# Kernel optimization log

Measured on AMD Instinct MI355X. Metric: run time of the kernel, lower is better.

Reference implementation:

```python
import jax, jax.numpy as jnp
import numpy as np

FP8_MAX = 448.0  # max representable magnitude of float8_e4m3fn
SCALE_EPS = 1e-7


def setup_inputs() -> dict:
    key = jax.random.key(0)
    k1, k2, k3 = jax.random.split(key, 3)
    in_f, out_f = 2048, 2048
    x = jax.random.normal(k1, (4, 4096, in_f), dtype=jnp.float32)
    # weight is stored in fp8 in the torch module; materialize fp8-representable fp32 values
    w_fp32 = jax.random.normal(k2, (out_f, in_f), dtype=jnp.float32) * (1.0 / np.sqrt(in_f))
    weight = w_fp32.astype(jnp.float8_e4m3fn).astype(jnp.float32)
    weight_scale = jnp.ones((), dtype=jnp.float32)
    bound = 1.0 / np.sqrt(in_f)
    bias = jax.random.uniform(k3, (out_f,), dtype=jnp.float32, minval=-bound, maxval=bound)
    return {"x": x, "weight": weight, "weight_scale": weight_scale, "bias": bias}


def reference(x, weight, weight_scale, bias):
    # per-tensor dynamic fp8 quantization of the input (scale = absmax / 448)
    scale = jnp.maximum(jnp.max(jnp.abs(x)) / FP8_MAX, SCALE_EPS)
    x_q = (x / scale).astype(jnp.float8_e4m3fn).astype(jnp.float32)
    # dequantize weight (fp8 values stored as fp32 here) with its per-tensor scale
    w = weight * weight_scale
    # NOTE: faithful to the source, the output is NOT rescaled by the input scale
    # (the original forward drops input_scale after quantization).
    out = jnp.einsum('bsi,oi->bso', x_q, w) + bias
    return out
```

## Files before the change

kernel.cpp:

```cpp
#include <hip/hip_runtime.h>
#include <hip/hip_bf16.h>

typedef __attribute__((ext_vector_type(4))) float floatx4;
typedef __attribute__((ext_vector_type(8))) int   intx8;

#define FP8_MAX_F 448.0f
#define SCALE_EPS 1e-7f

__global__ void k_absmax(const float* __restrict__ x, unsigned* __restrict__ amax, int n4) {
    __shared__ float wmax[4];
    int tid = blockIdx.x * blockDim.x + threadIdx.x;
    int stride = gridDim.x * blockDim.x;
    const float4* x4 = (const float4*)x;
    float m = 0.f;
    for (int i = tid; i < n4; i += stride) {
        float4 v = x4[i];
        m = fmaxf(fmaxf(fabsf(v.x), fabsf(v.y)),
                  fmaxf(m, fmaxf(fabsf(v.z), fabsf(v.w))));
    }
    #pragma unroll
    for (int off = 32; off > 0; off >>= 1) m = fmaxf(m, __shfl_xor(m, off, 64));
    if ((threadIdx.x & 63) == 0) wmax[threadIdx.x >> 6] = m;
    __syncthreads();
    if (threadIdx.x == 0) {
        float t = fmaxf(fmaxf(wmax[0], wmax[1]), fmaxf(wmax[2], wmax[3]));
        atomicMax(amax, __float_as_uint(t));
    }
}

__global__ void k_quant_w(const float* __restrict__ w, int* __restrict__ wq, int n16) {
    int tid = blockIdx.x * blockDim.x + threadIdx.x;
    int stride = gridDim.x * blockDim.x;
    const float4* x4 = (const float4*)w;
    int4* q4 = (int4*)wq;
    for (int i = tid; i < n16; i += stride) {
        float4 v0 = x4[4*i], v1 = x4[4*i+1], v2 = x4[4*i+2], v3 = x4[4*i+3];
        int4 o;
        o.x = __builtin_amdgcn_cvt_pk_fp8_f32(v0.x, v0.y, 0, false);
        o.x = __builtin_amdgcn_cvt_pk_fp8_f32(v0.z, v0.w, o.x, true);
        o.y = __builtin_amdgcn_cvt_pk_fp8_f32(v1.x, v1.y, 0, false);
        o.y = __builtin_amdgcn_cvt_pk_fp8_f32(v1.z, v1.w, o.y, true);
        o.z = __builtin_amdgcn_cvt_pk_fp8_f32(v2.x, v2.y, 0, false);
        o.z = __builtin_amdgcn_cvt_pk_fp8_f32(v2.z, v2.w, o.z, true);
        o.w = __builtin_amdgcn_cvt_pk_fp8_f32(v3.x, v3.y, 0, false);
        o.w = __builtin_amdgcn_cvt_pk_fp8_f32(v3.z, v3.w, o.w, true);
        q4[i] = o;
    }
}

__global__ void k_quant_x(const float* __restrict__ x, int* __restrict__ xq,
                          const unsigned* __restrict__ amax, int n16) {
    float scale = fmaxf(__uint_as_float(*amax) / FP8_MAX_F, SCALE_EPS);
    int tid = blockIdx.x * blockDim.x + threadIdx.x;
    int stride = gridDim.x * blockDim.x;
    const float4* x4 = (const float4*)x;
    int4* q4 = (int4*)xq;
    for (int i = tid; i < n16; i += stride) {
        float4 v0 = x4[4*i], v1 = x4[4*i+1], v2 = x4[4*i+2], v3 = x4[4*i+3];
        int4 o;
        o.x = __builtin_amdgcn_cvt_pk_fp8_f32(v0.x / scale, v0.y / scale, 0, false);
        o.x = __builtin_amdgcn_cvt_pk_fp8_f32(v0.z / scale, v0.w / scale, o.x, true);
        o.y = __builtin_amdgcn_cvt_pk_fp8_f32(v1.x / scale, v1.y / scale, 0, false);
        o.y = __builtin_amdgcn_cvt_pk_fp8_f32(v1.z / scale, v1.w / scale, o.y, true);
        o.z = __builtin_amdgcn_cvt_pk_fp8_f32(v2.x / scale, v2.y / scale, 0, false);
        o.z = __builtin_amdgcn_cvt_pk_fp8_f32(v2.z / scale, v2.w / scale, o.z, true);
        o.w = __builtin_amdgcn_cvt_pk_fp8_f32(v3.x / scale, v3.y / scale, 0, false);
        o.w = __builtin_amdgcn_cvt_pk_fp8_f32(v3.z / scale, v3.w / scale, o.w, true);
        q4[i] = o;
    }
}

#define BM 256
#define BN 256
#define BKQ 128
#define NT 16

#define GLOAD(src, dst) \
    __builtin_amdgcn_global_load_lds((const __attribute__((address_space(1))) void*)(src), \
                                     (__attribute__((address_space(3))) void*)(dst), 16, 0, 0)
#define BARRIER()   asm volatile("s_barrier" ::: "memory")
#define WAIT_VM(n)  asm volatile("s_waitcnt vmcnt(" #n ")" ::: "memory")
#define WAIT_LGKM(n) asm volatile("s_waitcnt lgkmcnt(" #n ")" ::: "memory")
#define SB0()       __builtin_amdgcn_sched_barrier(0)

#define LDFRAG(dstv, pL, pH, IMM) {                      \
    int4 lo_ = *(const int4*)((pL) + (IMM));             \
    int4 hi_ = *(const int4*)((pH) + (IMM));             \
    dstv = (intx8){lo_.x, lo_.y, lo_.z, lo_.w, hi_.x, hi_.y, hi_.z, hi_.w}; }

#define MFMA_ROW(m, af)                                                            \
    acc[m][0] = __builtin_amdgcn_mfma_scale_f32_16x16x128_f8f6f4(                  \
        af, b0, acc[m][0], 0, 0, 0, 0x7F7F7F7F, 0, 0x7F7F7F7F);                    \
    acc[m][1] = __builtin_amdgcn_mfma_scale_f32_16x16x128_f8f6f4(                  \
        af, b1, acc[m][1], 0, 0, 0, 0x7F7F7F7F, 0, 0x7F7F7F7F);                    \
    acc[m][2] = __builtin_amdgcn_mfma_scale_f32_16x16x128_f8f6f4(                  \
        af, b2, acc[m][2], 0, 0, 0, 0x7F7F7F7F, 0, 0x7F7F7F7F);                    \
    acc[m][3] = __builtin_amdgcn_mfma_scale_f32_16x16x128_f8f6f4(                  \
        af, b3, acc[m][3], 0, 0, 0, 0x7F7F7F7F, 0, 0x7F7F7F7F);

__global__ __launch_bounds__(512, 2) void k_gemm_mx(
    const unsigned char* __restrict__ A, const unsigned char* __restrict__ B,
    const float* __restrict__ bias, const float* __restrict__ wscale,
    float* __restrict__ C, int M, int N, int K) {
    __shared__ __align__(16) unsigned char lds[131072];

    int nwg = gridDim.x;
    int bid = blockIdx.x;
    bid = (bid & 7) * (nwg >> 3) + (bid >> 3);
    int ntn = N / BN;
    int tm = bid / ntn, tn = bid % ntn;
    int row0 = tm * BM, col0 = tn * BN;

    int tid = (int)threadIdx.x;
    int lane = tid & 63, wid = tid >> 6;
    int wr = wid >> 2, wc = wid & 3;
    int fr = lane & 15, g = lane >> 4;

    int srow = tid >> 3;
    int sc   = (tid & 7) ^ (srow & 7);
    const int offA0 = (row0 + srow) * K + sc * 16;
    const int offB0 = (col0 + srow) * K + sc * 16;
    unsigned char* dstA = lds + tid * 16;
    unsigned char* dstB = dstA + 32768;

    int c0 = (2 * g) ^ (fr & 7);
    const int aL = wr * 16384 + fr * 128 + c0 * 16;
    const int aH = wr * 16384 + fr * 128 + (c0 ^ 1) * 16;
    const int bL = 32768 + wc * 8192 + fr * 128 + c0 * 16;
    const int bH = 32768 + wc * 8192 + fr * 128 + (c0 ^ 1) * 16;

    floatx4 acc[8][4];
    #pragma unroll
    for (int m = 0; m < 8; ++m)
        #pragma unroll
        for (int n = 0; n < 4; ++n) acc[m][n] = (floatx4)(0.f);

    GLOAD(A + offA0,          dstA);
    GLOAD(A + offA0 + 131072, dstA + 8192);
    GLOAD(A + offA0 + 262144, dstA + 16384);
    GLOAD(A + offA0 + 393216, dstA + 24576);
    GLOAD(B + offB0,          dstB);
    GLOAD(B + offB0 + 131072, dstB + 8192);
    GLOAD(B + offB0 + 262144, dstB + 16384);
    GLOAD(B + offB0 + 393216, dstB + 24576);

    #pragma unroll 2
    for (int t = 0; t < NT; ++t) {
        const int bufo = (t & 1) << 16;
        const int nbufo = bufo ^ 65536;
        const unsigned char* AbL = lds + bufo + aL;
        const unsigned char* AbH = lds + bufo + aH;
        const unsigned char* BbL = lds + bufo + bL;
        const unsigned char* BbH = lds + bufo + bH;
        unsigned char* dA = dstA + nbufo;
        unsigned char* dB = dstB + nbufo;
        const int kn = ((t + 1) & (NT - 1)) * BKQ;

        GLOAD(A + kn + offA0,          dA);
        GLOAD(A + kn + offA0 + 131072, dA + 8192);
        GLOAD(A + kn + offA0 + 262144, dA + 16384);
        GLOAD(A + kn + offA0 + 393216, dA + 24576);
        GLOAD(B + kn + offB0,          dB);
        GLOAD(B + kn + offB0 + 131072, dB + 8192);
        GLOAD(B + kn + offB0 + 262144, dB + 16384);
        GLOAD(B + kn + offB0 + 393216, dB + 24576);
        SB0();
        WAIT_VM(8);
        SB0();
        BARRIER();

        intx8 b0, b1, b2, b3, aP0, aP1, aQ0, aQ1;
        LDFRAG(b0, BbL, BbH, 0)
        LDFRAG(b1, BbL, BbH, 2048)
        LDFRAG(b2, BbL, BbH, 4096)
        LDFRAG(b3, BbL, BbH, 6144)
        LDFRAG(aP0, AbL, AbH, 0)
        LDFRAG(aP1, AbL, AbH, 2048)
        LDFRAG(aQ0, AbL, AbH, 4096)
        LDFRAG(aQ1, AbL, AbH, 6144)
        SB0(); WAIT_LGKM(4); SB0();
        __builtin_amdgcn_s_setprio(1);
        MFMA_ROW(0, aP0)
        MFMA_ROW(1, aP1)
        __builtin_amdgcn_s_setprio(0);
        LDFRAG(aP0, AbL, AbH, 8192)
        LDFRAG(aP1, AbL, AbH, 10240)
        SB0(); WAIT_LGKM(4); SB0();
        __builtin_amdgcn_s_setprio(1);
        MFMA_ROW(2, aQ0)
        MFMA_ROW(3, aQ1)
        __builtin_amdgcn_s_setprio(0);
        LDFRAG(aQ0, AbL, AbH, 12288)
        LDFRAG(aQ1, AbL, AbH, 14336)
        SB0(); WAIT_LGKM(4); SB0();
        __builtin_amdgcn_s_setprio(1);
        MFMA_ROW(4, aP0)
        MFMA_ROW(5, aP1)
        __builtin_amdgcn_s_setprio(0);
        SB0(); WAIT_LGKM(0); SB0();
        __builtin_amdgcn_s_setprio(1);
        MFMA_ROW(6, aQ0)
        MFMA_ROW(7, aQ1)
        __builtin_amdgcn_s_setprio(0);
        BARRIER();
    }

    WAIT_VM(0);

    float wsv = *wscale;
    int crow = (lane >> 4) * 4;
    int ccol = lane & 15;
    float bv[4];
    #pragma unroll
    for (int n = 0; n < 4; ++n) bv[n] = bias[col0 + wc * 64 + n * 16 + ccol];
    #pragma unroll
    for (int m = 0; m < 8; ++m) {
        int r = row0 + wr * 128 + m * 16 + crow;
        #pragma unroll
        for (int n = 0; n < 4; ++n) {
            int c = col0 + wc * 64 + n * 16 + ccol;
            #pragma unroll
            for (int j = 0; j < 4; ++j)
                C[(long)(r + j) * N + c] = acc[m][n][j] * wsv + bv[n];
        }
    }
}

extern "C" void kernel_launch(void* const* d_in, const int* in_sizes, int n_in,
                              void* d_out, int out_size, void* d_ws, size_t ws_size,
                              hipStream_t stream) {
    const float* x      = (const float*)d_in[0];
    const float* w      = (const float*)d_in[1];
    const float* wscale = (const float*)d_in[2];
    const float* bias   = (const float*)d_in[3];
    float* out = (float*)d_out;

    const int K = 2048, N = 2048;
    const int M = in_sizes[0] / K;

    unsigned char* ws = (unsigned char*)d_ws;
    unsigned* amax = (unsigned*)ws;
    int* wq = (int*)(ws + 1024);
    int* xq = (int*)(ws + 1024 + (size_t)N * K);

    hipMemsetAsync(amax, 0, 4, stream);
    k_absmax<<<2048, 256, 0, stream>>>(x, amax, (M * K) / 4);
    k_quant_w<<<1024, 256, 0, stream>>>(w, wq, (N * K) / 16);
    k_quant_x<<<2048, 256, 0, stream>>>(x, xq, amax, (M * K) / 16);

    int grid = (M / BM) * (N / BN);
    k_gemm_mx<<<grid, 512, 0, stream>>>((const unsigned char*)xq, (const unsigned char*)wq,
                                        bias, wscale, out, M, N, K);
}
```

Measured before the change: 164.0 us.

## Fuse absmax and weight quant kernels; simplify GEMM inner loop scheduling

Merges the input absmax reduction and the weight fp8 conversion into a single launch, splitting blocks between the two jobs, so one kernel launch and its tail are removed. Separately, the GEMM main loop drops its hand-tuned interleaving of LDS fragment loads with MFMA groups, along with the sched barriers, lgkmcnt waits, setprio hints and the unroll-2 pragma. All A fragments are now loaded up front and scheduling is left to the compiler. This raises register pressure and may lose the overlap between LDS reads and MFMAs.

```diff
diff --git a/kernel.cpp b/kernel.cpp
--- a/kernel.cpp
+++ b/kernel.cpp
@@ -7,44 +7,45 @@
 #define FP8_MAX_F 448.0f
 #define SCALE_EPS 1e-7f
 
-__global__ void k_absmax(const float* __restrict__ x, unsigned* __restrict__ amax, int n4) {
-    __shared__ float wmax[4];
-    int tid = blockIdx.x * blockDim.x + threadIdx.x;
-    int stride = gridDim.x * blockDim.x;
-    const float4* x4 = (const float4*)x;
-    float m = 0.f;
-    for (int i = tid; i < n4; i += stride) {
-        float4 v = x4[i];
-        m = fmaxf(fmaxf(fabsf(v.x), fabsf(v.y)),
-                  fmaxf(m, fmaxf(fabsf(v.z), fabsf(v.w))));
-    }
-    #pragma unroll
-    for (int off = 32; off > 0; off >>= 1) m = fmaxf(m, __shfl_xor(m, off, 64));
-    if ((threadIdx.x & 63) == 0) wmax[threadIdx.x >> 6] = m;
-    __syncthreads();
-    if (threadIdx.x == 0) {
-        float t = fmaxf(fmaxf(wmax[0], wmax[1]), fmaxf(wmax[2], wmax[3]));
-        atomicMax(amax, __float_as_uint(t));
-    }
-}
-
-__global__ void k_quant_w(const float* __restrict__ w, int* __restrict__ wq, int n16) {
-    int tid = blockIdx.x * blockDim.x + threadIdx.x;
-    int stride = gridDim.x * blockDim.x;
-    const float4* x4 = (const float4*)w;
-    int4* q4 = (int4*)wq;
-    for (int i = tid; i < n16; i += stride) {
-        float4 v0 = x4[4*i], v1 = x4[4*i+1], v2 = x4[4*i+2], v3 = x4[4*i+3];
-        int4 o;
-        o.x = __builtin_amdgcn_cvt_pk_fp8_f32(v0.x, v0.y, 0, false);
-        o.x = __builtin_amdgcn_cvt_pk_fp8_f32(v0.z, v0.w, o.x, true);
-        o.y = __builtin_amdgcn_cvt_pk_fp8_f32(v1.x, v1.y, 0, false);
-        o.y = __builtin_amdgcn_cvt_pk_fp8_f32(v1.z, v1.w, o.y, true);
-        o.z = __builtin_amdgcn_cvt_pk_fp8_f32(v2.x, v2.y, 0, false);
-        o.z = __builtin_amdgcn_cvt_pk_fp8_f32(v2.z, v2.w, o.z, true);
-        o.w = __builtin_amdgcn_cvt_pk_fp8_f32(v3.x, v3.y, 0, false);
-        o.w = __builtin_amdgcn_cvt_pk_fp8_f32(v3.z, v3.w, o.w, true);
-        q4[i] = o;
+__global__ void k_pre(const float* __restrict__ x, unsigned* __restrict__ amax, int n4,
+                      const float* __restrict__ w, int* __restrict__ wq, int nw16) {
+    if (blockIdx.x < 1792) {
+        __shared__ float wmax[4];
+        int tid = blockIdx.x * 256 + threadIdx.x;
+        int stride = 1792 * 256;
+        const float4* x4 = (const float4*)x;
+        float m = 0.f;
+        for (int i = tid; i < n4; i += stride) {
+            float4 v = x4[i];
+            m = fmaxf(fmaxf(fabsf(v.x), fabsf(v.y)),
+                      fmaxf(m, fmaxf(fabsf(v.z), fabsf(v.w))));
+        }
+        #pragma unroll
+        for (int off = 32; off > 0; off >>= 1) m = fmaxf(m, __shfl_xor(m, off, 64));
+        if ((threadIdx.x & 63) == 0) wmax[threadIdx.x >> 6] = m;
+        __syncthreads();
+        if (threadIdx.x == 0) {
+            float t = fmaxf(fmaxf(wmax[0], wmax[1]), fmaxf(wmax[2], wmax[3]));
+            atomicMax(amax, __float_as_uint(t));
+        }
+    } else {
+        int tid = (blockIdx.x - 1792) * 256 + threadIdx.x;
+        int stride = 256 * 256;
+        const float4* x4 = (const float4*)w;
+        int4* q4 = (int4*)wq;
+        for (int i = tid; i < nw16; i += stride) {
+            float4 v0 = x4[4*i], v1 = x4[4*i+1], v2 = x4[4*i+2], v3 = x4[4*i+3];
+            int4 o;
+            o.x = __builtin_amdgcn_cvt_pk_fp8_f32(v0.x, v0.y, 0, false);
+            o.x = __builtin_amdgcn_cvt_pk_fp8_f32(v0.z, v0.w, o.x, true);
+            o.y = __builtin_amdgcn_cvt_pk_fp8_f32(v1.x, v1.y, 0, false);
+            o.y = __builtin_amdgcn_cvt_pk_fp8_f32(v1.z, v1.w, o.y, true);
+            o.z = __builtin_amdgcn_cvt_pk_fp8_f32(v2.x, v2.y, 0, false);
+            o.z = __builtin_amdgcn_cvt_pk_fp8_f32(v2.z, v2.w, o.z, true);
+            o.w = __builtin_amdgcn_cvt_pk_fp8_f32(v3.x, v3.y, 0, false);
+            o.w = __builtin_amdgcn_cvt_pk_fp8_f32(v3.z, v3.w, o.w, true);
+            q4[i] = o;
+        }
     }
 }
 
@@ -80,8 +81,6 @@
                                      (__attribute__((address_space(3))) void*)(dst), 16, 0, 0)
 #define BARRIER()   asm volatile("s_barrier" ::: "memory")
 #define WAIT_VM(n)  asm volatile("s_waitcnt vmcnt(" #n ")" ::: "memory")
-#define WAIT_LGKM(n) asm volatile("s_waitcnt lgkmcnt(" #n ")" ::: "memory")
-#define SB0()       __builtin_amdgcn_sched_barrier(0)
 
 #define LDFRAG(dstv, pL, pH, IMM) {                      \
     int4 lo_ = *(const int4*)((pL) + (IMM));             \
@@ -144,7 +143,6 @@
     GLOAD(B + offB0 + 262144, dstB + 16384);
     GLOAD(B + offB0 + 393216, dstB + 24576);
 
-    #pragma unroll 2
     for (int t = 0; t < NT; ++t) {
         const int bufo = (t & 1) << 16;
         const int nbufo = bufo ^ 65536;
@@ -164,44 +162,30 @@
         GLOAD(B + kn + offB0 + 131072, dB + 8192);
         GLOAD(B + kn + offB0 + 262144, dB + 16384);
         GLOAD(B + kn + offB0 + 393216, dB + 24576);
-        SB0();
         WAIT_VM(8);
-        SB0();
         BARRIER();
 
-        intx8 b0, b1, b2, b3, aP0, aP1, aQ0, aQ1;
+        intx8 b0, b1, b2, b3, a0, a1, a2, a3, a4, a5, a6, a7;
         LDFRAG(b0, BbL, BbH, 0)
         LDFRAG(b1, BbL, BbH, 2048)
         LDFRAG(b2, BbL, BbH, 4096)
         LDFRAG(b3, BbL, BbH, 6144)
-        LDFRAG(aP0, AbL, AbH, 0)
-        LDFRAG(aP1, AbL, AbH, 2048)
-        LDFRAG(aQ0, AbL, AbH, 4096)
-        LDFRAG(aQ1, AbL, AbH, 6144)
-        SB0(); WAIT_LGKM(4); SB0();
-        __builtin_amdgcn_s_setprio(1);
-        MFMA_ROW(0, aP0)
-        MFMA_ROW(1, aP1)
-        __builtin_amdgcn_s_setprio(0);
-        LDFRAG(aP0, AbL, AbH, 8192)
-        LDFRAG(aP1, AbL, AbH, 10240)
-        SB0(); WAIT_LGKM(4); SB0();
-        __builtin_amdgcn_s_setprio(1);
-        MFMA_ROW(2, aQ0)
-        MFMA_ROW(3, aQ1)
-        __builtin_amdgcn_s_setprio(0);
-        LDFRAG(aQ0, AbL, AbH, 12288)
-        LDFRAG(aQ1, AbL, AbH, 14336)
-        SB0(); WAIT_LGKM(4); SB0();
-        __builtin_amdgcn_s_setprio(1);
-        MFMA_ROW(4, aP0)
-        MFMA_ROW(5, aP1)
-        __builtin_amdgcn_s_setprio(0);
-        SB0(); WAIT_LGKM(0); SB0();
-        __builtin_amdgcn_s_setprio(1);
-        MFMA_ROW(6, aQ0)
-        MFMA_ROW(7, aQ1)
-        __builtin_amdgcn_s_setprio(0);
+        LDFRAG(a0, AbL, AbH, 0)
+        LDFRAG(a1, AbL, AbH, 2048)
+        LDFRAG(a2, AbL, AbH, 4096)
+        LDFRAG(a3, AbL, AbH, 6144)
+        LDFRAG(a4, AbL, AbH, 8192)
+        LDFRAG(a5, AbL, AbH, 10240)
+        LDFRAG(a6, AbL, AbH, 12288)
+        LDFRAG(a7, AbL, AbH, 14336)
+        MFMA_ROW(0, a0)
+        MFMA_ROW(1, a1)
+        MFMA_ROW(2, a2)
+        MFMA_ROW(3, a3)
+        MFMA_ROW(4, a4)
+        MFMA_ROW(5, a5)
+        MFMA_ROW(6, a6)
+        MFMA_ROW(7, a7)
         BARRIER();
     }
 
@@ -244,8 +228,7 @@
     int* xq = (int*)(ws + 1024 + (size_t)N * K);
 
     hipMemsetAsync(amax, 0, 4, stream);
-    k_absmax<<<2048, 256, 0, stream>>>(x, amax, (M * K) / 4);
-    k_quant_w<<<1024, 256, 0, stream>>>(w, wq, (N * K) / 16);
+    k_pre<<<2048, 256, 0, stream>>>(x, amax, (M * K) / 4, w, wq, (N * K) / 16);
     k_quant_x<<<2048, 256, 0, stream>>>(x, xq, amax, (M * K) / 16);
 
     int grid = (M / BM) * (N / BN);
```

New measurement: 149.3 us. 9.0% less time.
